# Performance work log

Measured on AMD Instinct MI355X. Metric: run time of the kernel, lower is better.

The kernel has to match this reference:

```python
import jax, jax.numpy as jnp
import numpy as np

N, S, E = 8, 2048, 512
H, D = 8, 64            # heads, head_dim
P = 16                  # num_persistent
ALIBI_ALPHA = 1.0
START_I = 0


def setup_inputs() -> dict:
    key = jax.random.key(0)
    ks = jax.random.split(key, 12)
    inp = {
        "values": jax.random.normal(ks[0], (N, S, E), jnp.float32),
        "keys": jax.random.normal(ks[1], (N, S, E), jnp.float32),
        "queries": jax.random.normal(ks[2], (N, S, E), jnp.float32),
        "mask": jax.random.randint(ks[3], (N, 1, S, S), 0, 2, jnp.int32),
        # per-head-dim projections (torch Linear, no bias): weight shape (out, in)
        "Wv": jax.random.normal(ks[4], (D, D), jnp.float32) / np.sqrt(D),
        "Wk": jax.random.normal(ks[5], (D, D), jnp.float32) / np.sqrt(D),
        "Wq": jax.random.normal(ks[6], (D, D), jnp.float32) / np.sqrt(D),
        "Wo": jax.random.normal(ks[7], (E, E), jnp.float32) / np.sqrt(E),
        "bo": jnp.zeros((E,), jnp.float32),
        # talking-heads 1x1 conv weights, squeezed to (H_out, H_in)
        "pre_th": jax.random.normal(ks[8], (H, H), jnp.float32) / np.sqrt(H),
        "post_th": jax.random.normal(ks[9], (H, H), jnp.float32) / np.sqrt(H),
        # persistent memory tokens (P, H, D)
        "pk": jax.random.normal(ks[10], (P, H, D), jnp.float32) * 0.1,
        "pv": jax.random.normal(ks[11], (P, H, D), jnp.float32) * 0.1,
    }
    return inp


def reference(values, keys, queries, mask, Wv, Wk, Wq, Wo, bo, pre_th, post_th, pk, pv):
    n, q_len, e = queries.shape
    k_len = keys.shape[1]
    h, d = pk.shape[1], pk.shape[2]

    # split heads: [n, s, h, d]
    v = values.reshape(n, -1, h, d)
    k = keys.reshape(n, -1, h, d)
    q = queries.reshape(n, -1, h, d)

    # per-head-dim linear projections (torch: x @ W.T)
    v = jnp.einsum('nshd,ed->nshe', v, Wv)
    k = jnp.einsum('nshd,ed->nshe', k, Wk)
    q = jnp.einsum('nshd,ed->nshe', q, Wq)

    # append persistent memory tokens along key/value sequence dim
    p = pk.shape[0]
    k = jnp.concatenate([k, jnp.broadcast_to(pk[None], (n, p, h, d))], axis=1)
    v = jnp.concatenate([v, jnp.broadcast_to(pv[None], (n, p, h, d))], axis=1)

    # energy: [n, h, q, k_len + p]
    energy = jnp.einsum('nqhd,nkhd->nhqk', q, k)

    # ALiBi bias: -|i - j| * slope_h, zero bias on persistent slots
    slopes = 2.0 ** (-ALIBI_ALPHA * (jnp.arange(1, h + 1, dtype=jnp.float32) + START_I))
    t_q = jnp.arange(q_len)
    t_k = jnp.arange(k_len)
    dist = jnp.abs(t_q[:, None] - t_k[None, :]).astype(jnp.float32)  # [q, k]
    alibi = -dist[None, None] * slopes[None, :, None, None]          # [1, h, q, k]
    alibi = jnp.pad(alibi, ((0, 0), (0, 0), (0, 0), (0, p)))
    energy = energy + alibi

    # pre-softmax talking heads (1x1 conv over head channel)
    energy = jnp.einsum('ij,njqk->niqk', pre_th, energy)

    # mask (pad persistent slots with 1 = keep)
    mask_p = jnp.pad(mask, ((0, 0), (0, 0), (0, 0), (0, p)), constant_values=1)
    energy = jnp.where(mask_p == 0, jnp.float32(-1e4), energy)

    attn = jax.nn.softmax(energy / jnp.sqrt(jnp.float32(e)), axis=3)

    # post-softmax talking heads
    attn = jnp.einsum('ij,njqk->niqk', post_th, attn)

    out = jnp.einsum('nhql,nlhd->nqhd', attn, v).reshape(n, q_len, e)
    out = out @ Wo.T + bo
    return out
```

## Files before the change

### kernel.cpp

```cpp
#include <hip/hip_runtime.h>

#define N_ 8
#define S_ 2048
#define E_ 512
#define KL_ 2064
#define NTT_ 65
#define VTSZ 1064960
#define SCALE2 0.063758723f
#define NEGBIG -700.0f

typedef unsigned short u16;
typedef unsigned int u32;
typedef __attribute__((ext_vector_type(2))) float f32x2;
typedef __attribute__((ext_vector_type(4))) float f32x4;
typedef __attribute__((ext_vector_type(4))) short bf16x4;
typedef __attribute__((ext_vector_type(8))) short bf16x8;

__device__ __forceinline__ u16 f2bf(float x) {
  u32 u = __float_as_uint(x);
  u32 r = (u + 0x7FFFu + ((u >> 16) & 1u)) >> 16;
  return (u16)r;
}

__device__ __forceinline__ float exp2_fast(float x) {
  float r;
  asm("v_exp_f32 %0, %1" : "=v"(r) : "v"(x));
  return r;
}

__device__ __forceinline__ f32x4 mfma16(bf16x4 a, bf16x4 b, f32x4 c) {
#if __has_builtin(__builtin_amdgcn_mfma_f32_16x16x16bf16_1k)
  return __builtin_amdgcn_mfma_f32_16x16x16bf16_1k(a, b, c, 0, 0, 0);
#else
  f32x4 d;
  asm("v_mfma_f32_16x16x16_bf16 %0, %1, %2, %3" : "=v"(d) : "v"(a), "v"(b), "v"(c));
  return d;
#endif
}

__device__ __forceinline__ void gload_lds16(const void* g, void* l) {
  __builtin_amdgcn_global_load_lds((const __attribute__((address_space(1))) unsigned int*)g,
                                   (__attribute__((address_space(3))) unsigned int*)l, 16, 0, 0);
}

__global__ __launch_bounds__(256) void maskpack_kernel(const int* __restrict__ mask,
                                                       u32* __restrict__ bm) {
  const int t = threadIdx.x;
  const int w = t >> 6, lane = t & 63;
  const int blk = blockIdx.x;
  const int n = blk >> 9;
  const int qrow = ((blk & 511) << 2) + w;
  const int* row = mask + ((size_t)n * S_ + qrow) * S_;
  __shared__ u32 tl[4][64];
  u32 myword = 0;
  #pragma unroll 4
  for (int k = 0; k < 32; ++k) {
    int v = row[k * 64 + lane];
    unsigned long long b = __ballot(v != 0);
    if ((lane >> 1) == k) myword = (lane & 1) ? (u32)(b >> 32) : (u32)b;
  }
  tl[w][lane] = myword;
  __syncthreads();
  const int qq = t & 3, wi = t >> 2;
  const int qb = ((blk & 511) << 2) + qq;
  bm[((size_t)n * 64 + wi) * S_ + qb] = tl[qq][wi];
}

__global__ __launch_bounds__(256, 2) void proj_kernel(
    const float* __restrict__ V_, const float* __restrict__ K_, const float* __restrict__ Q_,
    const float* __restrict__ Wv, const float* __restrict__ Wk, const float* __restrict__ Wq,
    u16* __restrict__ Kp, u16* __restrict__ Qp, u16* __restrict__ VT) {
  __shared__ u16 xt[64 * 512];
  __shared__ u16 wt[64 * 64];
  const int tz = blockIdx.y;
  const float* X = (tz == 0) ? V_ : (tz == 1) ? K_ : Q_;
  const float* W = (tz == 0) ? Wv : (tz == 1) ? Wk : Wq;
  const int t = threadIdx.x, lane = t & 63, w = t >> 6, g = lane >> 4, li = lane & 15;
  const int rb = blockIdx.x * 64;
  const int nn = rb >> 11, sb = rb & 2047;

  for (int c = t; c < 512; c += 256) {
    int r = c >> 3, s = c & 7;
    float4 a = *(const float4*)&W[r * 64 + s * 8];
    float4 b = *(const float4*)&W[r * 64 + s * 8 + 4];
    bf16x8 v = {(short)f2bf(a.x), (short)f2bf(a.y), (short)f2bf(a.z), (short)f2bf(a.w),
                (short)f2bf(b.x), (short)f2bf(b.y), (short)f2bf(b.z), (short)f2bf(b.w)};
    *(bf16x8*)&wt[r * 64 + ((s ^ (r & 7)) * 8)] = v;
  }
  for (int c = t; c < 4096; c += 256) {
    int r = c >> 6, s = c & 63;
    const float* src = &X[(size_t)(rb + r) * 512 + s * 8];
    float4 a = *(const float4*)src;
    float4 b = *(const float4*)(src + 4);
    bf16x8 v = {(short)f2bf(a.x), (short)f2bf(a.y), (short)f2bf(a.z), (short)f2bf(a.w),
                (short)f2bf(b.x), (short)f2bf(b.y), (short)f2bf(b.z), (short)f2bf(b.w)};
    *(bf16x8*)&xt[r * 512 + ((s ^ (r & 7)) * 8)] = v;
  }
  __syncthreads();

  bf16x8 fx[8][2];
  #pragma unroll
  for (int h = 0; h < 8; ++h)
    #pragma unroll
    for (int dh = 0; dh < 2; ++dh) {
      int row = w * 16 + li;
      fx[h][dh] = *(const bf16x8*)&xt[row * 512 + (((h * 8 + dh * 4 + g) ^ (row & 7)) * 8)];
    }
  bf16x8 fw[4][2];
  #pragma unroll
  for (int c = 0; c < 4; ++c)
    #pragma unroll
    for (int dh = 0; dh < 2; ++dh) {
      int row = c * 16 + li;
      fw[c][dh] = *(const bf16x8*)&wt[row * 64 + (((dh * 4 + g) ^ (row & 7)) * 8)];
    }

  f32x4 C[8][4];
  #pragma unroll
  for (int h = 0; h < 8; ++h)
    #pragma unroll
    for (int c = 0; c < 4; ++c) C[h][c] = (f32x4){0.f, 0.f, 0.f, 0.f};

  if (tz == 0) {
    #pragma unroll
    for (int h = 0; h < 8; ++h)
      #pragma unroll
      for (int dh = 0; dh < 2; ++dh)
        #pragma unroll
        for (int c = 0; c < 4; ++c)
          C[h][c] = __builtin_amdgcn_mfma_f32_16x16x32_bf16(fw[c][dh], fx[h][dh], C[h][c], 0, 0, 0);
    #pragma unroll
    for (int h = 0; h < 8; ++h)
      #pragma unroll
      for (int c = 0; c < 4; ++c)
        #pragma unroll
        for (int r = 0; r < 4; ++r) {
          int e = h * 64 + c * 16 + g * 4 + r;
          int l = sb + w * 16 + li;
          VT[(((size_t)nn * 65 + (l >> 5)) * 512 + e) * 32 + (l & 31)] = f2bf(C[h][c][r]);
        }
  } else {
    #pragma unroll
    for (int h = 0; h < 8; ++h)
      #pragma unroll
      for (int dh = 0; dh < 2; ++dh)
        #pragma unroll
        for (int c = 0; c < 4; ++c)
          C[h][c] = __builtin_amdgcn_mfma_f32_16x16x32_bf16(fx[h][dh], fw[c][dh], C[h][c], 0, 0, 0);
    #pragma unroll
    for (int h = 0; h < 8; ++h)
      #pragma unroll
      for (int c = 0; c < 4; ++c)
        #pragma unroll
        for (int r = 0; r < 4; ++r) {
          int e = h * 64 + c * 16 + li;
          u16 val = f2bf(C[h][c][r]);
          if (tz == 2) Qp[(size_t)(rb + w * 16 + g * 4 + r) * 512 + e] = val;
          else Kp[((size_t)nn * KL_ + sb + w * 16 + g * 4 + r) * 512 + e] = val;
        }
  }
}

__global__ __launch_bounds__(256) void persist_kernel(const float* __restrict__ pk,
                                                      const float* __restrict__ pv,
                                                      u16* __restrict__ Kp, u16* __restrict__ VT) {
  int id = blockIdx.x * 256 + threadIdx.x;
  if (id < 65536) {
    int n = id >> 13, p = (id >> 9) & 15, e = id & 511;
    Kp[((size_t)n * KL_ + S_ + p) * 512 + e] = f2bf(pk[p * 512 + e]);
  } else {
    int rem = id - 65536;
    int n = rem >> 14, p = (rem >> 9) & 31, e = rem & 511;
    u16 val = (p < 16) ? f2bf(pv[p * 512 + e]) : (u16)0;
    VT[(((size_t)n * 65 + 64) * 512 + e) * 32 + p] = val;
  }
}

__global__ __launch_bounds__(512, 2) void attn_kernel(
    const u16* __restrict__ Qp, const u16* __restrict__ Kp, const u16* __restrict__ VT,
    const u32* __restrict__ bm, const float* __restrict__ pre_th,
    const float* __restrict__ post_th, u16* __restrict__ Ohb) {
  __shared__ __align__(16) char smem[151552];
  u16* KtB = (u16*)smem;
  u16* VtB = (u16*)(smem + 65536);
  u32* mlds = (u32*)(smem + 131072);
  float* Zbuf = (float*)(smem + 147456);

  const int t = threadIdx.x, lane = t & 63, w = t >> 6, g = lane >> 4, li = lane & 15;
  const int qw = w & 3, lh = w >> 2;
  const int bid = blockIdx.x;
  const int n = bid & 7;
  const int q0 = (bid >> 3) * 64;
  const int myq = q0 + qw * 16 + li;
  const float myq_f = (float)myq;

  const u16* Kbase = Kp + (size_t)n * KL_ * 512;
  const u16* Vbase = VT + (size_t)n * VTSZ;

  #define STAGE_K(buf, tile) {                                                          \
    _Pragma("unroll")                                                                   \
    for (int i_ = 0; i_ < 4; ++i_) {                                                    \
      int row_ = w + i_ * 8;                                                            \
      gload_lds16(Kbase + (size_t)((tile) * 32 + row_) * 512 + ((lane ^ (row_ & 7)) * 8),\
                  KtB + (buf) * 16384 + row_ * 512);                                    \
    } }
  #define STAGE_V(buf, tile) {                                                          \
    _Pragma("unroll")                                                                   \
    for (int i_ = 0; i_ < 4; ++i_) {                                                    \
      int c_ = t + i_ * 512;                                                            \
      int e_ = c_ >> 2, q16_ = c_ & 3;                                                  \
      gload_lds16(Vbase + (size_t)(tile) * 16384 + e_ * 32 + ((q16_ ^ (e_ & 3)) * 8),   \
                  VtB + (buf) * 16384 + (i_ * 512 + w * 64) * 8);                       \
    } }

  for (int idx = t; idx < 4096; idx += 512)
    mlds[idx] = bm[((size_t)n * 64 + (idx >> 6)) * S_ + q0 + (idx & 63)];

  bf16x8 qf[8][2];
  {
    const u16* qrow = Qp + (size_t)(n * S_ + myq) * 512;
    #pragma unroll
    for (int h = 0; h < 8; ++h)
      #pragma unroll
      for (int dh = 0; dh < 2; ++dh)
        qf[h][dh] = *(const bf16x8*)(qrow + h * 64 + dh * 32 + g * 8);
  }
  float nms[8];
  #pragma unroll
  for (int i = 0; i < 8; ++i) {
    float a = 0.f;
    #pragma unroll
    for (int j = 0; j < 8; ++j) a += pre_th[i * 8 + j] * exp2f(-(float)(j + 1));
    nms[i] = -a * SCALE2;
  }

  float Zr[8];
  #pragma unroll
  for (int i = 0; i < 8; ++i) Zr[i] = 0.f;

  STAGE_K(0, 0)
  __syncthreads();

  for (int tt = 0; tt < NTT_; ++tt) {
    if (tt + 1 < NTT_) STAGE_K((tt + 1) & 1, tt + 1)
    __builtin_amdgcn_sched_barrier(0);
    const u16* kb = KtB + (tt & 1) * 16384;
    f32x4 C[8];
    #pragma unroll
    for (int h = 0; h < 8; ++h) C[h] = (f32x4){0.f, 0.f, 0.f, 0.f};
    #pragma unroll
    for (int h = 0; h < 8; ++h)
      #pragma unroll
      for (int dh = 0; dh < 2; ++dh) {
        bf16x8 a = *(const bf16x8*)(kb + (lh * 16 + li) * 512 + (((h * 8 + dh * 4 + g) ^ (li & 7)) * 8));
        C[h] = __builtin_amdgcn_mfma_f32_16x16x32_bf16(a, qf[h][dh], C[h], 0, 0, 0);
      }
    u32 mbits;
    float dist[4];
    const int l0 = tt * 32 + lh * 16 + g * 4;
    if (tt < 64) {
      mbits = (mlds[tt * 64 + qw * 16 + li] >> (lh * 16 + g * 4)) & 0xFu;
      #pragma unroll
      for (int r = 0; r < 4; ++r) dist[r] = fabsf(myq_f - (float)(l0 + r));
    } else {
      mbits = (lh == 0) ? 0xFu : 0u;
      #pragma unroll
      for (int r = 0; r < 4; ++r) dist[r] = 0.f;
    }
    f32x2 accl[8], acch[8];
    #pragma unroll
    for (int i = 0; i < 8; ++i) { accl[i] = (f32x2){0.f, 0.f}; acch[i] = (f32x2){0.f, 0.f}; }
    #pragma unroll
    for (int j = 0; j < 8; ++j) {
      f32x2 elo = {C[j].x, C[j].y}, ehi = {C[j].z, C[j].w};
      #pragma unroll
      for (int i = 0; i < 8; ++i) {
        float p = pre_th[i * 8 + j];
        accl[i] += p * elo; acch[i] += p * ehi;
      }
    }
    const bool al = (tt < 64);
    #pragma unroll
    for (int i = 0; i < 8; ++i) {
      float t0 = fmaf(accl[i].x, SCALE2, -64.f);
      float t1 = fmaf(accl[i].y, SCALE2, -64.f);
      float t2 = fmaf(acch[i].x, SCALE2, -64.f);
      float t3 = fmaf(acch[i].y, SCALE2, -64.f);
      if (al) {
        t0 = fmaf(dist[0], nms[i], t0); t1 = fmaf(dist[1], nms[i], t1);
        t2 = fmaf(dist[2], nms[i], t2); t3 = fmaf(dist[3], nms[i], t3);
      }
      t0 = (mbits & 1u) ? t0 : NEGBIG; t1 = (mbits & 2u) ? t1 : NEGBIG;
      t2 = (mbits & 4u) ? t2 : NEGBIG; t3 = (mbits & 8u) ? t3 : NEGBIG;
      Zr[i] += (exp2_fast(t0) + exp2_fast(t1)) + (exp2_fast(t2) + exp2_fast(t3));
    }
    asm volatile("s_waitcnt vmcnt(0)" ::: "memory");
    __builtin_amdgcn_s_barrier();
  }

  STAGE_K(0, 0)
  STAGE_V(0, 0)
  __builtin_amdgcn_sched_barrier(0);

  #pragma unroll
  for (int i = 0; i < 8; ++i) {
    Zr[i] += __shfl_xor(Zr[i], 16);
    Zr[i] += __shfl_xor(Zr[i], 32);
  }
  if (lane < 16) {
    #pragma unroll
    for (int i = 0; i < 8; ++i) Zbuf[(lh * 64 + qw * 16 + li) * 8 + i] = Zr[i];
  }
  __syncthreads();
  float nm1[8];
  #pragma unroll
  for (int i = 0; i < 8; ++i) {
    float zt = Zbuf[(qw * 16 + li) * 8 + i] + Zbuf[(64 + qw * 16 + li) * 8 + i];
    nm1[i] = -(64.f + __log2f(zt));
  }

  f32x4 O[8][4];
  #pragma unroll
  for (int o = 0; o < 8; ++o)
    #pragma unroll
    for (int dc = 0; dc < 4; ++dc) O[o][dc] = (f32x4){0.f, 0.f, 0.f, 0.f};

  const int cloff = (((lh * 2 + (g >> 1)) ^ (li & 3)) * 8) + (g & 1) * 4;

  for (int tt = 0; tt < NTT_; ++tt) {
    if (tt + 1 < NTT_) { STAGE_K((tt + 1) & 1, tt + 1) STAGE_V((tt + 1) & 1, tt + 1) }
    __builtin_amdgcn_sched_barrier(0);
    const u16* kb = KtB + (tt & 1) * 16384;
    const u16* vb = VtB + (tt & 1) * 16384;
    f32x4 C[8];
    #pragma unroll
    for (int h = 0; h < 8; ++h) C[h] = (f32x4){0.f, 0.f, 0.f, 0.f};
    #pragma unroll
    for (int h = 0; h < 8; ++h)
      #pragma unroll
      for (int dh = 0; dh < 2; ++dh) {
        bf16x8 a = *(const bf16x8*)(kb + (lh * 16 + li) * 512 + (((h * 8 + dh * 4 + g) ^ (li & 7)) * 8));
        C[h] = __builtin_amdgcn_mfma_f32_16x16x32_bf16(a, qf[h][dh], C[h], 0, 0, 0);
      }
    u32 mbits;
    float dist[4];
    const int l0 = tt * 32 + lh * 16 + g * 4;
    if (tt < 64) {
      mbits = (mlds[tt * 64 + qw * 16 + li] >> (lh * 16 + g * 4)) & 0xFu;
      #pragma unroll
      for (int r = 0; r < 4; ++r) dist[r] = fabsf(myq_f - (float)(l0 + r));
    } else {
      mbits = (lh == 0) ? 0xFu : 0u;
      #pragma unroll
      for (int r = 0; r < 4; ++r) dist[r] = 0.f;
    }
    f32x2 accl[8], acch[8];
    #pragma unroll
    for (int i = 0; i < 8; ++i) { accl[i] = (f32x2){0.f, 0.f}; acch[i] = (f32x2){0.f, 0.f}; }
    #pragma unroll
    for (int j = 0; j < 8; ++j) {
      f32x2 elo = {C[j].x, C[j].y}, ehi = {C[j].z, C[j].w};
      #pragma unroll
      for (int i = 0; i < 8; ++i) {
        float p = pre_th[i * 8 + j];
        accl[i] += p * elo; acch[i] += p * ehi;
      }
    }
    const bool al = (tt < 64);
    f32x2 ppl[8], pph[8];
    #pragma unroll
    for (int i = 0; i < 8; ++i) {
      float t0 = fmaf(accl[i].x, SCALE2, nm1[i]);
      float t1 = fmaf(accl[i].y, SCALE2, nm1[i]);
      float t2 = fmaf(acch[i].x, SCALE2, nm1[i]);
      float t3 = fmaf(acch[i].y, SCALE2, nm1[i]);
      if (al) {
        t0 = fmaf(dist[0], nms[i], t0); t1 = fmaf(dist[1], nms[i], t1);
        t2 = fmaf(dist[2], nms[i], t2); t3 = fmaf(dist[3], nms[i], t3);
      }
      t0 = (mbits & 1u) ? t0 : NEGBIG; t1 = (mbits & 2u) ? t1 : NEGBIG;
      t2 = (mbits & 4u) ? t2 : NEGBIG; t3 = (mbits & 8u) ? t3 : NEGBIG;
      ppl[i] = (f32x2){exp2_fast(t0), exp2_fast(t1)};
      pph[i] = (f32x2){exp2_fast(t2), exp2_fast(t3)};
    }
    f32x2 pol[8], poh[8];
    #pragma unroll
    for (int o = 0; o < 8; ++o) { pol[o] = (f32x2){0.f, 0.f}; poh[o] = (f32x2){0.f, 0.f}; }
    #pragma unroll
    for (int i = 0; i < 8; ++i) {
      #pragma unroll
      for (int o = 0; o < 8; ++o) {
        float c = post_th[o * 8 + i];
        pol[o] += c * ppl[i]; poh[o] += c * pph[i];
      }
    }
    #pragma unroll
    for (int o = 0; o < 8; ++o) {
      bf16x4 pa = {(short)f2bf(pol[o].x), (short)f2bf(pol[o].y),
                   (short)f2bf(poh[o].x), (short)f2bf(poh[o].y)};
      #pragma unroll
      for (int dc = 0; dc < 4; ++dc) {
        int e = o * 64 + dc * 16 + li;
        bf16x4 b = *(const bf16x4*)(vb + e * 32 + cloff);
        O[o][dc] = mfma16(pa, b, O[o][dc]);
      }
    }
    asm volatile("s_waitcnt vmcnt(0)" ::: "memory");
    __builtin_amdgcn_s_barrier();
  }

  float* ep = (float*)smem;
  if (lh == 1) {
    #pragma unroll
    for (int o = 0; o < 8; ++o)
      #pragma unroll
      for (int dc = 0; dc < 4; ++dc)
        *(f32x4*)&ep[qw * 8192 + ((o * 4 + dc) * 64 + li * 4 + g) * 4] = O[o][dc];
  }
  __syncthreads();
  if (lh == 0) {
    u16* dst = Ohb + (size_t)(n * S_ + q0 + qw * 16) * 512;
    #pragma unroll
    for (int o = 0; o < 8; ++o)
      #pragma unroll
      for (int dc = 0; dc < 4; ++dc) {
        f32x4 oth = *(const f32x4*)&ep[qw * 8192 + ((o * 4 + dc) * 64 + li * 4 + g) * 4];
        f32x4 v = O[o][dc] + oth;
        int e = o * 64 + dc * 16 + li;
        #pragma unroll
        for (int r = 0; r < 4; ++r) dst[(size_t)(g * 4 + r) * 512 + e] = f2bf(v[r]);
      }
  }
  #undef STAGE_K
  #undef STAGE_V
}

__global__ __launch_bounds__(256) void out_proj_kernel(
    const u16* __restrict__ Ohb, const float* __restrict__ Wo,
    const float* __restrict__ bo, float* __restrict__ out) {
  __shared__ __align__(16) u16 As[2][128 * 32];
  __shared__ __align__(16) u16 Bs[2][128 * 32];
  const int t = threadIdx.x, lane = t & 63, w = t >> 6, g = lane >> 4, li = lane & 15;
  const int wq = w & 1, wp = w >> 1;
  const int r0 = blockIdx.y * 128, c0 = blockIdx.x * 128;

  #define STAGE_A(buf, ks) {                                                  \
    _Pragma("unroll")                                                         \
    for (int i_ = 0; i_ < 2; ++i_) {                                          \
      int c_ = t + i_ * 256;                                                  \
      gload_lds16(Ohb + (size_t)(r0 + (c_ >> 2)) * 512 + (ks) + (c_ & 3) * 8, \
                  &As[buf][(i_ * 256 + w * 64) * 8]);                         \
    } }
  #define STAGE_B(buf, ks) {                                                  \
    _Pragma("unroll")                                                         \
    for (int i_ = 0; i_ < 2; ++i_) {                                          \
      int c_ = t + i_ * 256;                                                  \
      const float* s_ = &Wo[(size_t)(c0 + (c_ >> 2)) * 512 + (ks) + (c_ & 3) * 8]; \
      float4 a_ = *(const float4*)s_;                                         \
      float4 b_ = *(const float4*)(s_ + 4);                                   \
      bf16x8 v_ = {(short)f2bf(a_.x), (short)f2bf(a_.y), (short)f2bf(a_.z), (short)f2bf(a_.w), \
                   (short)f2bf(b_.x), (short)f2bf(b_.y), (short)f2bf(b_.z), (short)f2bf(b_.w)}; \
      *(bf16x8*)&Bs[buf][c_ * 8] = v_;                                        \
    } }

  f32x4 acc[4][4];
  #pragma unroll
  for (int m = 0; m < 4; ++m)
    #pragma unroll
    for (int nn = 0; nn < 4; ++nn) acc[m][nn] = (f32x4){0.f, 0.f, 0.f, 0.f};

  STAGE_A(0, 0)
  STAGE_B(0, 0)
  __syncthreads();
  for (int s = 0; s < 16; ++s) {
    if (s + 1 < 16) { STAGE_A((s + 1) & 1, (s + 1) * 32) STAGE_B((s + 1) & 1, (s + 1) * 32) }
    const u16* ab = As[s & 1];
    const u16* bb = Bs[s & 1];
    bf16x8 af[4], bf[4];
    #pragma unroll
    for (int m = 0; m < 4; ++m) af[m] = *(const bf16x8*)(ab + (wp * 64 + m * 16 + li) * 32 + g * 8);
    #pragma unroll
    for (int nn = 0; nn < 4; ++nn) bf[nn] = *(const bf16x8*)(bb + (wq * 64 + nn * 16 + li) * 32 + g * 8);
    #pragma unroll
    for (int m = 0; m < 4; ++m)
      #pragma unroll
      for (int nn = 0; nn < 4; ++nn)
        acc[m][nn] = __builtin_amdgcn_mfma_f32_16x16x32_bf16(af[m], bf[nn], acc[m][nn], 0, 0, 0);
    __syncthreads();
  }
  #pragma unroll
  for (int nn = 0; nn < 4; ++nn) {
    int col = c0 + wq * 64 + nn * 16 + li;
    float bv = bo[col];
    #pragma unroll
    for (int m = 0; m < 4; ++m)
      #pragma unroll
      for (int r = 0; r < 4; ++r)
        out[(size_t)(r0 + wp * 64 + m * 16 + g * 4 + r) * 512 + col] = acc[m][nn][r] + bv;
  }
  #undef STAGE_A
  #undef STAGE_B
}

extern "C" void kernel_launch(void* const* d_in, const int* in_sizes, int n_in,
                              void* d_out, int out_size, void* d_ws, size_t ws_size,
                              hipStream_t stream) {
  const float* values  = (const float*)d_in[0];
  const float* keys    = (const float*)d_in[1];
  const float* queries = (const float*)d_in[2];
  const int*   mask    = (const int*)d_in[3];
  const float* Wv      = (const float*)d_in[4];
  const float* Wk      = (const float*)d_in[5];
  const float* Wq      = (const float*)d_in[6];
  const float* Wo      = (const float*)d_in[7];
  const float* bo      = (const float*)d_in[8];
  const float* pre_th  = (const float*)d_in[9];
  const float* post_th = (const float*)d_in[10];
  const float* pk      = (const float*)d_in[11];
  const float* pv      = (const float*)d_in[12];

  char* ws = (char*)d_ws;
  u16*  Qp  = (u16*)ws;
  u16*  Kp  = (u16*)(ws + 16777216);
  u16*  VT  = (u16*)(ws + 33685504);
  u16*  Ohb = (u16*)(ws + 50724864);
  u32*  bm  = (u32*)(ws + 67502080);

  hipLaunchKernelGGL(maskpack_kernel, dim3(4096), dim3(256), 0, stream, mask, bm);
  hipLaunchKernelGGL(proj_kernel, dim3(256, 3), dim3(256), 0, stream,
                     values, keys, queries, Wv, Wk, Wq, Kp, Qp, VT);
  hipLaunchKernelGGL(persist_kernel, dim3(768), dim3(256), 0, stream, pk, pv, Kp, VT);
  hipLaunchKernelGGL(attn_kernel, dim3(256), dim3(512), 0, stream,
                     Qp, Kp, VT, bm, pre_th, post_th, Ohb);
  hipLaunchKernelGGL(out_proj_kernel, dim3(4, 128), dim3(256), 0, stream,
                     Ohb, Wo, bo, (float*)d_out);
}
```

Baseline: 911.3 us.

## Split softmax normalizer pass into separate split-K kernel with more blocks

The first pass of the attention kernel, which computes the softmax denominators Z, becomes its own z_kernel. That kernel splits the key tiles into two halves across 512 blocks with a higher occupancy bound and writes partial Z to a workspace buffer. The PV kernel reads and sums the two partials instead of recomputing them. This spreads the Z pass over more workgroups to improve GPU fill, but it adds an extra launch, a global round trip for Z, and reloads Q and mask in both kernels.

```diff
diff --git a/kernel.cpp b/kernel.cpp
--- a/kernel.cpp
+++ b/kernel.cpp
@@ -176,15 +176,145 @@
   }
 }
 
-__global__ __launch_bounds__(512, 2) void attn_kernel(
+__global__ __launch_bounds__(512, 4) void z_kernel(
+    const u16* __restrict__ Qp, const u16* __restrict__ Kp,
+    const u32* __restrict__ bm, const float* __restrict__ pre_th,
+    float* __restrict__ Zp) {
+  __shared__ __align__(16) u16 KtB[2][32 * 512];
+  __shared__ u32 mlds[33 * 64];
+  __shared__ float Zbuf[2 * 64 * 8];
+
+  const int t = threadIdx.x, lane = t & 63, w = t >> 6, g = lane >> 4, li = lane & 15;
+  const int qw = w & 3, lh = w >> 2;
+  const int bid = blockIdx.x;
+  const int n = bid & 7;
+  const int rem = bid >> 3;
+  const int qb = rem >> 1, kh = rem & 1;
+  const int q0 = qb * 64;
+  const int tb = kh ? 33 : 0;
+  const int nt = kh ? 32 : 33;
+  const int wc = kh ? 31 : 33;
+  const int myq = q0 + qw * 16 + li;
+  const float myq_f = (float)myq;
+
+  const u16* Kbase = Kp + (size_t)n * KL_ * 512;
+
+  #define ZSTAGE_K(buf, tile) {                                                         \
+    _Pragma("unroll")                                                                   \
+    for (int i_ = 0; i_ < 4; ++i_) {                                                    \
+      int row_ = w + i_ * 8;                                                            \
+      gload_lds16(Kbase + (size_t)((tile) * 32 + row_) * 512 + ((lane ^ (row_ & 7)) * 8),\
+                  &KtB[buf][row_ * 512]);                                               \
+    } }
+
+  for (int idx = t; idx < wc * 64; idx += 512)
+    mlds[idx] = bm[((size_t)n * 64 + tb + (idx >> 6)) * S_ + q0 + (idx & 63)];
+
+  bf16x8 qf[8][2];
+  {
+    const u16* qrow = Qp + (size_t)(n * S_ + myq) * 512;
+    #pragma unroll
+    for (int h = 0; h < 8; ++h)
+      #pragma unroll
+      for (int dh = 0; dh < 2; ++dh)
+        qf[h][dh] = *(const bf16x8*)(qrow + h * 64 + dh * 32 + g * 8);
+  }
+  float nms[8];
+  #pragma unroll
+  for (int i = 0; i < 8; ++i) {
+    float a = 0.f;
+    #pragma unroll
+    for (int j = 0; j < 8; ++j) a += pre_th[i * 8 + j] * exp2f(-(float)(j + 1));
+    nms[i] = -a * SCALE2;
+  }
+
+  float Zr[8];
+  #pragma unroll
+  for (int i = 0; i < 8; ++i) Zr[i] = 0.f;
+
+  ZSTAGE_K(0, tb)
+  __syncthreads();
+
+  for (int j = 0; j < nt; ++j) {
+    const int tile = tb + j;
+    if (j + 1 < nt) ZSTAGE_K((j + 1) & 1, tb + j + 1)
+    __builtin_amdgcn_sched_barrier(0);
+    const u16* kb = &KtB[j & 1][0];
+    f32x4 C[8];
+    #pragma unroll
+    for (int h = 0; h < 8; ++h) C[h] = (f32x4){0.f, 0.f, 0.f, 0.f};
+    #pragma unroll
+    for (int h = 0; h < 8; ++h)
+      #pragma unroll
+      for (int dh = 0; dh < 2; ++dh) {
+        bf16x8 a = *(const bf16x8*)(kb + (lh * 16 + li) * 512 + (((h * 8 + dh * 4 + g) ^ (li & 7)) * 8));
+        C[h] = __builtin_amdgcn_mfma_f32_16x16x32_bf16(a, qf[h][dh], C[h], 0, 0, 0);
+      }
+    u32 mbits;
+    float dist[4];
+    const int l0 = tile * 32 + lh * 16 + g * 4;
+    if (tile < 64) {
+      mbits = (mlds[j * 64 + qw * 16 + li] >> (lh * 16 + g * 4)) & 0xFu;
+      #pragma unroll
+      for (int r = 0; r < 4; ++r) dist[r] = fabsf(myq_f - (float)(l0 + r));
+    } else {
+      mbits = (lh == 0) ? 0xFu : 0u;
+      #pragma unroll
+      for (int r = 0; r < 4; ++r) dist[r] = 0.f;
+    }
+    const bool al = (tile < 64);
+    #pragma unroll
+    for (int i = 0; i < 8; ++i) {
+      f32x2 al2 = (f32x2){0.f, 0.f}, ah2 = (f32x2){0.f, 0.f};
+      #pragma unroll
+      for (int j2 = 0; j2 < 8; ++j2) {
+        float p = pre_th[i * 8 + j2];
+        al2 += p * (f32x2){C[j2].x, C[j2].y};
+        ah2 += p * (f32x2){C[j2].z, C[j2].w};
+      }
+      float t0 = fmaf(al2.x, SCALE2, -64.f);
+      float t1 = fmaf(al2.y, SCALE2, -64.f);
+      float t2 = fmaf(ah2.x, SCALE2, -64.f);
+      float t3 = fmaf(ah2.y, SCALE2, -64.f);
+      if (al) {
+        t0 = fmaf(dist[0], nms[i], t0); t1 = fmaf(dist[1], nms[i], t1);
+        t2 = fmaf(dist[2], nms[i], t2); t3 = fmaf(dist[3], nms[i], t3);
+      }
+      t0 = (mbits & 1u) ? t0 : NEGBIG; t1 = (mbits & 2u) ? t1 : NEGBIG;
+      t2 = (mbits & 4u) ? t2 : NEGBIG; t3 = (mbits & 8u) ? t3 : NEGBIG;
+      Zr[i] += (exp2_fast(t0) + exp2_fast(t1)) + (exp2_fast(t2) + exp2_fast(t3));
+    }
+    asm volatile("s_waitcnt vmcnt(0)" ::: "memory");
+    __builtin_amdgcn_s_barrier();
+  }
+
+  #pragma unroll
+  for (int i = 0; i < 8; ++i) {
+    Zr[i] += __shfl_xor(Zr[i], 16);
+    Zr[i] += __shfl_xor(Zr[i], 32);
+  }
+  if (lane < 16) {
+    #pragma unroll
+    for (int i = 0; i < 8; ++i) Zbuf[(lh * 64 + qw * 16 + li) * 8 + i] = Zr[i];
+  }
+  __syncthreads();
+  {
+    int q = t >> 3, i = t & 7;
+    float val = Zbuf[q * 8 + i] + Zbuf[(64 + q) * 8 + i];
+    Zp[((size_t)(kh * 8 + n) * 2048 + q0 + q) * 8 + i] = val;
+  }
+  #undef ZSTAGE_K
+}
+
+__global__ __launch_bounds__(512, 2) void pv_kernel(
     const u16* __restrict__ Qp, const u16* __restrict__ Kp, const u16* __restrict__ VT,
     const u32* __restrict__ bm, const float* __restrict__ pre_th,
-    const float* __restrict__ post_th, u16* __restrict__ Ohb) {
+    const float* __restrict__ post_th, const float* __restrict__ Zp,
+    u16* __restrict__ Ohb) {
   __shared__ __align__(16) char smem[151552];
   u16* KtB = (u16*)smem;
   u16* VtB = (u16*)(smem + 65536);
   u32* mlds = (u32*)(smem + 131072);
-  float* Zbuf = (float*)(smem + 147456);
 
   const int t = threadIdx.x, lane = t & 63, w = t >> 6, g = lane >> 4, li = lane & 15;
   const int qw = w & 3, lh = w >> 2;
@@ -233,99 +363,25 @@
     for (int j = 0; j < 8; ++j) a += pre_th[i * 8 + j] * exp2f(-(float)(j + 1));
     nms[i] = -a * SCALE2;
   }
-
-  float Zr[8];
-  #pragma unroll
-  for (int i = 0; i < 8; ++i) Zr[i] = 0.f;
-
-  STAGE_K(0, 0)
-  __syncthreads();
-
-  for (int tt = 0; tt < NTT_; ++tt) {
-    if (tt + 1 < NTT_) STAGE_K((tt + 1) & 1, tt + 1)
-    __builtin_amdgcn_sched_barrier(0);
-    const u16* kb = KtB + (tt & 1) * 16384;
-    f32x4 C[8];
-    #pragma unroll
-    for (int h = 0; h < 8; ++h) C[h] = (f32x4){0.f, 0.f, 0.f, 0.f};
-    #pragma unroll
-    for (int h = 0; h < 8; ++h)
-      #pragma unroll
-      for (int dh = 0; dh < 2; ++dh) {
-        bf16x8 a = *(const bf16x8*)(kb + (lh * 16 + li) * 512 + (((h * 8 + dh * 4 + g) ^ (li & 7)) * 8));
-        C[h] = __builtin_amdgcn_mfma_f32_16x16x32_bf16(a, qf[h][dh], C[h], 0, 0, 0);
-      }
-    u32 mbits;
-    float dist[4];
-    const int l0 = tt * 32 + lh * 16 + g * 4;
-    if (tt < 64) {
-      mbits = (mlds[tt * 64 + qw * 16 + li] >> (lh * 16 + g * 4)) & 0xFu;
-      #pragma unroll
-      for (int r = 0; r < 4; ++r) dist[r] = fabsf(myq_f - (float)(l0 + r));
-    } else {
-      mbits = (lh == 0) ? 0xFu : 0u;
-      #pragma unroll
-      for (int r = 0; r < 4; ++r) dist[r] = 0.f;
-    }
-    f32x2 accl[8], acch[8];
-    #pragma unroll
-    for (int i = 0; i < 8; ++i) { accl[i] = (f32x2){0.f, 0.f}; acch[i] = (f32x2){0.f, 0.f}; }
-    #pragma unroll
-    for (int j = 0; j < 8; ++j) {
-      f32x2 elo = {C[j].x, C[j].y}, ehi = {C[j].z, C[j].w};
-      #pragma unroll
-      for (int i = 0; i < 8; ++i) {
-        float p = pre_th[i * 8 + j];
-        accl[i] += p * elo; acch[i] += p * ehi;
-      }
-    }
-    const bool al = (tt < 64);
-    #pragma unroll
-    for (int i = 0; i < 8; ++i) {
-      float t0 = fmaf(accl[i].x, SCALE2, -64.f);
-      float t1 = fmaf(accl[i].y, SCALE2, -64.f);
-      float t2 = fmaf(acch[i].x, SCALE2, -64.f);
-      float t3 = fmaf(acch[i].y, SCALE2, -64.f);
-      if (al) {
-        t0 = fmaf(dist[0], nms[i], t0); t1 = fmaf(dist[1], nms[i], t1);
-        t2 = fmaf(dist[2], nms[i], t2); t3 = fmaf(dist[3], nms[i], t3);
-      }
-      t0 = (mbits & 1u) ? t0 : NEGBIG; t1 = (mbits & 2u) ? t1 : NEGBIG;
-      t2 = (mbits & 4u) ? t2 : NEGBIG; t3 = (mbits & 8u) ? t3 : NEGBIG;
-      Zr[i] += (exp2_fast(t0) + exp2_fast(t1)) + (exp2_fast(t2) + exp2_fast(t3));
-    }
-    asm volatile("s_waitcnt vmcnt(0)" ::: "memory");
-    __builtin_amdgcn_s_barrier();
-  }
+  float nm1[8];
+  {
+    const float* zp0 = Zp + ((size_t)n * 2048 + myq) * 8;
+    const float* zp1 = Zp + ((size_t)(8 + n) * 2048 + myq) * 8;
+    #pragma unroll
+    for (int i = 0; i < 8; ++i) nm1[i] = -(64.f + __log2f(zp0[i] + zp1[i]));
+  }
+
+  f32x4 O[8][4];
+  #pragma unroll
+  for (int o = 0; o < 8; ++o)
+    #pragma unroll
+    for (int dc = 0; dc < 4; ++dc) O[o][dc] = (f32x4){0.f, 0.f, 0.f, 0.f};
+
+  const int cloff = (((lh * 2 + (g >> 1)) ^ (li & 3)) * 8) + (g & 1) * 4;
 
   STAGE_K(0, 0)
   STAGE_V(0, 0)
-  __builtin_amdgcn_sched_barrier(0);
-
-  #pragma unroll
-  for (int i = 0; i < 8; ++i) {
-    Zr[i] += __shfl_xor(Zr[i], 16);
-    Zr[i] += __shfl_xor(Zr[i], 32);
-  }
-  if (lane < 16) {
-    #pragma unroll
-    for (int i = 0; i < 8; ++i) Zbuf[(lh * 64 + qw * 16 + li) * 8 + i] = Zr[i];
-  }
-  __syncthreads();
-  float nm1[8];
-  #pragma unroll
-  for (int i = 0; i < 8; ++i) {
-    float zt = Zbuf[(qw * 16 + li) * 8 + i] + Zbuf[(64 + qw * 16 + li) * 8 + i];
-    nm1[i] = -(64.f + __log2f(zt));
-  }
-
-  f32x4 O[8][4];
-  #pragma unroll
-  for (int o = 0; o < 8; ++o)
-    #pragma unroll
-    for (int dc = 0; dc < 4; ++dc) O[o][dc] = (f32x4){0.f, 0.f, 0.f, 0.f};
-
-  const int cloff = (((lh * 2 + (g >> 1)) ^ (li & 3)) * 8) + (g & 1) * 4;
+  __syncthreads();
 
   for (int tt = 0; tt < NTT_; ++tt) {
     if (tt + 1 < NTT_) { STAGE_K((tt + 1) & 1, tt + 1) STAGE_V((tt + 1) & 1, tt + 1) }
@@ -525,13 +581,16 @@
   u16*  VT  = (u16*)(ws + 33685504);
   u16*  Ohb = (u16*)(ws + 50724864);
   u32*  bm  = (u32*)(ws + 67502080);
+  float* Zp = (float*)(ws + 71696384);
 
   hipLaunchKernelGGL(maskpack_kernel, dim3(4096), dim3(256), 0, stream, mask, bm);
   hipLaunchKernelGGL(proj_kernel, dim3(256, 3), dim3(256), 0, stream,
                      values, keys, queries, Wv, Wk, Wq, Kp, Qp, VT);
   hipLaunchKernelGGL(persist_kernel, dim3(768), dim3(256), 0, stream, pk, pv, Kp, VT);
-  hipLaunchKernelGGL(attn_kernel, dim3(256), dim3(512), 0, stream,
-                     Qp, Kp, VT, bm, pre_th, post_th, Ohb);
+  hipLaunchKernelGGL(z_kernel, dim3(512), dim3(512), 0, stream,
+                     Qp, Kp, bm, pre_th, Zp);
+  hipLaunchKernelGGL(pv_kernel, dim3(256), dim3(512), 0, stream,
+                     Qp, Kp, VT, bm, pre_th, post_th, Zp, Ohb);
   hipLaunchKernelGGL(out_proj_kernel, dim3(4, 128), dim3(256), 0, stream,
                      Ohb, Wo, bo, (float*)d_out);
 }
```

After: 971.6 us. 6.6% more time.
